# Performance work log

Hardware: AMD Instinct MI355X
Metric: run time of the kernel (lower is better)

Reference implementation:

```python
import jax, jax.numpy as jnp
import numpy as np

N = 8192; E = 131072; K = 20; IN_DIM = 3; HID = 256; N_CLASSES = 32


def setup_inputs():
    key = jax.random.key(0)
    ks = jax.random.split(key, 16)

    def w(k, shape):
        lim = 1.0 / np.sqrt(shape[0])
        return jax.random.uniform(k, shape, jnp.float32, -lim, lim)

    f32 = jnp.float32
    return {
        "features": jax.random.normal(ks[0], (N, IN_DIM), f32),
        "src": jax.random.randint(ks[1], (E,), 0, N, jnp.int32),
        "dst": jax.random.randint(ks[2], (E,), 0, N, jnp.int32),
        # GraphConv params
        "Wc1": w(ks[3], (IN_DIM, HID)), "bc1": jnp.zeros((HID,), f32),
        "Wc2": w(ks[4], (HID, HID)), "bc2": jnp.zeros((HID,), f32),
        "Wc3": w(ks[5], (64, N_CLASSES)), "bc3": jnp.zeros((N_CLASSES,), f32),
        # DynamicEdgeConv 1 MLP: [2*256 -> 256 -> 256], Linear+BN+ReLU each
        "W11": w(ks[6], (2 * HID, 256)), "b11": jnp.zeros((256,), f32), "g11": jnp.ones((256,), f32), "be11": jnp.zeros((256,), f32),
        "W12": w(ks[7], (256, 256)), "b12": jnp.zeros((256,), f32), "g12": jnp.ones((256,), f32), "be12": jnp.zeros((256,), f32),
        # DynamicEdgeConv 2 MLP: [2*256 -> 64 -> 64]
        "W21": w(ks[8], (2 * 256, 64)), "b21": jnp.zeros((64,), f32), "g21": jnp.ones((64,), f32), "be21": jnp.zeros((64,), f32),
        "W22": w(ks[9], (64, 64)), "b22": jnp.zeros((64,), f32), "g22": jnp.ones((64,), f32), "be22": jnp.zeros((64,), f32),
    }


def reference(features, src, dst, Wc1, bc1, Wc2, bc2, Wc3, bc3,
              W11, b11, g11, be11, W12, b12, g12, be12,
              W21, b21, g21, be21, W22, b22, g22, be22):
    n = features.shape[0]
    ones_e = jnp.ones(src.shape[0], features.dtype)
    # DGL GraphConv norm='both': deg clamped to min 1
    dout = jnp.clip(jax.ops.segment_sum(ones_e, src, num_segments=n), 1.0) ** -0.5
    din = jnp.clip(jax.ops.segment_sum(ones_e, dst, num_segments=n), 1.0) ** -0.5

    def gconv(x, W, b, act):
        agg = jax.ops.segment_sum((x * dout[:, None])[src], dst, num_segments=n)
        r = (agg * din[:, None]) @ W + b
        return jax.nn.relu(r) if act else r

    def bn(x, g, b):  # BatchNorm1d in training mode over all edge rows
        mu = jnp.mean(x, axis=(0, 1), keepdims=True)
        var = jnp.mean(jnp.square(x - mu), axis=(0, 1), keepdims=True)
        return (x - mu) * jax.lax.rsqrt(var + 1e-5) * g + b

    def edge_conv(x, layers):
        # dynamic kNN graph on current features (self included, dist 0)
        sq = jnp.sum(x * x, axis=-1)
        d = sq[:, None] + sq[None, :] - 2.0 * (x @ x.T)  # [N,N]
        idx = jax.lax.top_k(-d, K)[1]                    # [N,K]
        xi = x[:, None, :]
        e = jnp.concatenate([jnp.broadcast_to(xi, (n, K, x.shape[-1])), x[idx] - xi], axis=-1)  # [N,K,2F]
        for W, b, g, be in layers:
            e = jax.nn.relu(bn(e @ W + b, g, be))
        return jnp.max(e, axis=1)  # max aggregation over neighbors

    h = gconv(features, Wc1, bc1, True)                                   # [N,256]
    h = edge_conv(h, [(W11, b11, g11, be11), (W12, b12, g12, be12)])      # [N,256]
    h = gconv(h, Wc2, bc2, True)                                          # [N,256]
    h = edge_conv(h, [(W21, b21, g21, be21), (W22, b22, g22, be22)])      # [N,64]
    return gconv(h, Wc3, bc3, False)                                      # [N,32]
```

## Files before the change

kernel.cpp:

```cpp
#include <hip/hip_runtime.h>

#define NN 8192
#define NE 131072
#define KNN 20
#define CH 4096
#define GBM 128
#define GBN 128
#define GBK 64

typedef __attribute__((ext_vector_type(4))) float f32x4;
typedef __attribute__((ext_vector_type(8))) __bf16 bf16x8;

__global__ void k_zero(float* p, int n){
  int i = blockIdx.x*256 + threadIdx.x;
  if (i < n) p[i] = 0.f;
}
__global__ void k_zero_i(int* p, int n){
  int i = blockIdx.x*256 + threadIdx.x;
  if (i < n) p[i] = 0;
}

__device__ __forceinline__ unsigned short f2bf(float x){
  unsigned u = __float_as_uint(x);
  unsigned r = (u + 0x7fff + ((u >> 16) & 1)) >> 16;
  return (unsigned short)r;
}
__device__ __forceinline__ float bf2f(unsigned short h){
  return __uint_as_float((unsigned)h << 16);
}
__device__ __forceinline__ void gload16(const void* g, void* l){
  __builtin_amdgcn_global_load_lds(
      (const __attribute__((address_space(1))) void*)g,
      (__attribute__((address_space(3))) void*)l, 16, 0, 0);
}
__device__ __forceinline__ unsigned mapu(float v){
  unsigned b = __float_as_uint(v);
  return b ^ (((unsigned)((int)b >> 31)) | 0x80000000u);
}
__device__ __forceinline__ float unmapu(unsigned u){
  unsigned b = (u & 0x80000000u) ? (u ^ 0x80000000u) : ~u;
  return __uint_as_float(b);
}

__global__ void k_count(const int* __restrict__ src, const int* __restrict__ dst,
                        int* cs, int* cd){
  int e = blockIdx.x*256 + threadIdx.x;
  if (e < NE){ atomicAdd(&cs[src[e]], 1); atomicAdd(&cd[dst[e]], 1); }
}
__global__ void k_deg(const int* cs, const int* cd, float* dout, float* din){
  int i = blockIdx.x*256 + threadIdx.x;
  if (i < NN){
    dout[i] = rsqrtf((float)max(cs[i], 1));
    din[i]  = rsqrtf((float)max(cd[i], 1));
  }
}
__global__ void k_scan(const int* __restrict__ cnt, int* __restrict__ off){
  __shared__ int sh[256];
  __shared__ int carry;
  int tid = threadIdx.x;
  if (tid == 0) carry = 0;
  __syncthreads();
  for (int base = 0; base < NN; base += 256){
    int v = cnt[base + tid];
    int x = v;
    sh[tid] = x; __syncthreads();
    for (int o = 1; o < 256; o <<= 1){
      int y = (tid >= o) ? sh[tid - o] : 0;
      __syncthreads();
      x += y; sh[tid] = x;
      __syncthreads();
    }
    off[base + tid] = carry + x - v;
    __syncthreads();
    if (tid == 255){
      carry += x;
      if (base + 256 == NN) off[NN] = carry;
    }
    __syncthreads();
  }
}
__global__ void k_fill(const int* __restrict__ src, const int* __restrict__ dst,
                       const int* __restrict__ roff, int* cursor, int* csr){
  int e = blockIdx.x*256 + threadIdx.x;
  if (e < NE){
    int d = dst[e];
    int p = atomicAdd(&cursor[d], 1);
    csr[roff[d] + p] = src[e];
  }
}

__global__ void k_gconv1(const float* __restrict__ feat, const int* __restrict__ roff,
                         const int* __restrict__ csr, const float* __restrict__ dout,
                         const float* __restrict__ din, const float* __restrict__ Wc1,
                         const float* __restrict__ bc1, float* __restrict__ h1){
  int wid = threadIdx.x >> 6, lane = threadIdx.x & 63;
  int i = blockIdx.x*4 + wid;
  float a0=0.f, a1=0.f, a2=0.f;
  int beg = roff[i], end = roff[i+1];
  for (int t = beg + lane; t < end; t += 64){
    int s = csr[t]; float w = dout[s];
    a0 += feat[s*3+0]*w; a1 += feat[s*3+1]*w; a2 += feat[s*3+2]*w;
  }
  for (int m = 32; m; m >>= 1){
    a0 += __shfl_xor(a0, m); a1 += __shfl_xor(a1, m); a2 += __shfl_xor(a2, m);
  }
  float dn = din[i];
  a0 *= dn; a1 *= dn; a2 *= dn;
  for (int c = lane; c < 256; c += 64){
    float r = a0*Wc1[c] + a1*Wc1[256+c] + a2*Wc1[512+c] + bc1[c];
    h1[(size_t)i*256 + c] = fmaxf(r, 0.f);
  }
}

__global__ void k_sq(const float* __restrict__ X, float* __restrict__ sq){
  int wid = threadIdx.x >> 6, lane = threadIdx.x & 63;
  int i = blockIdx.x*4 + wid;
  float4 v = *(const float4*)&X[(size_t)i*256 + lane*4];
  float s = v.x*v.x + v.y*v.y + v.z*v.z + v.w*v.w;
  for (int m = 32; m; m >>= 1) s += __shfl_xor(s, m);
  if (lane == 0) sq[i] = s;
}

__global__ void k_split(const float* __restrict__ X, unsigned short* __restrict__ xcat){
  int row = blockIdx.x, c = threadIdx.x;
  float x = X[(size_t)row*256 + c];
  unsigned short h = f2bf(x);
  unsigned short lo = f2bf(x - bf2f(h));
  xcat[(size_t)row*512 + c] = h;
  xcat[(size_t)row*512 + 256 + c] = lo;
}

__global__ void k_wsplit(const float* __restrict__ W, unsigned short* __restrict__ Whi,
                         unsigned short* __restrict__ Wlo){
  int k = blockIdx.x, n = threadIdx.x;
  float x = W[(size_t)k*256 + n];
  unsigned short h = f2bf(x);
  Whi[(size_t)n*256 + k] = h;
  Wlo[(size_t)n*256 + k] = f2bf(x - bf2f(h));
}
__global__ void k_wsplit64(const float* __restrict__ W, unsigned short* __restrict__ Whi,
                           unsigned short* __restrict__ Wlo){
  int k = blockIdx.x, n = threadIdx.x;
  float x = W[(size_t)k*64 + n];
  unsigned short h = f2bf(x);
  Whi[(size_t)n*64 + k] = h;
  Wlo[(size_t)n*64 + k] = f2bf(x - bf2f(h));
}

__global__ __launch_bounds__(256)
void k_gram_mfma(const unsigned short* __restrict__ Xcat, const float* __restrict__ sq,
                 float* __restrict__ G, int r0){
  __shared__ unsigned short sA[GBM*GBK];
  __shared__ unsigned short sB[GBM*GBK];
  __shared__ float sqr[GBM];
  __shared__ float sqc[GBN];
  int tid = threadIdx.x;
  int lw = tid >> 6, l = tid & 63;
  int rbl = blockIdx.y*GBM;
  int rb = r0 + rbl;
  int cb = blockIdx.x*GBN;

  if (tid < GBM) sqr[tid] = sq[rb + tid];
  else if (tid < GBM + GBN) sqc[tid - GBM] = sq[cb + tid - GBM];

  int srow = l >> 3;
  int scol = (l & 7) ^ srow;
  const unsigned short* srcA[4];
  const unsigned short* srcB[4];
  char* dstA[4]; char* dstB[4];
  #pragma unroll
  for (int i = 0; i < 4; i++){
    int c = lw*4 + i;
    int row = c*8 + srow;
    srcA[i] = Xcat + (size_t)(rb + row)*512 + scol*8;
    srcB[i] = Xcat + (size_t)(cb + row)*512 + scol*8;
    dstA[i] = (char*)sA + c*1024;
    dstB[i] = (char*)sB + c*1024;
  }

  int wm = lw >> 1, wn = lw & 1;
  int fm = l & 15, kg = l >> 4;
  unsigned offA[4][2], offB[4][2];
  #pragma unroll
  for (int mf = 0; mf < 4; mf++){
    int rowa = wm*64 + mf*16 + fm;
    int rowb = wn*64 + mf*16 + fm;
    #pragma unroll
    for (int ks = 0; ks < 2; ks++){
      offA[mf][ks] = rowa*128 + (((unsigned)(ks*4 + kg) ^ (rowa & 7)))*16;
      offB[mf][ks] = rowb*128 + (((unsigned)(ks*4 + kg) ^ (rowb & 7)))*16;
    }
  }

  f32x4 acc[4][4];
  #pragma unroll
  for (int m = 0; m < 4; m++)
    #pragma unroll
    for (int n = 0; n < 4; n++) acc[m][n] = (f32x4){0.f,0.f,0.f,0.f};

  #pragma unroll
  for (int s = 0; s < 12; s++){
    int sec = s >> 2;
    int inner = (s & 3)*64;
    int cbA = (sec == 1 ? 256 : 0) + inner;
    int cbB = (sec == 2 ? 256 : 0) + inner;
    #pragma unroll
    for (int i = 0; i < 4; i++){
      gload16(srcA[i] + cbA, dstA[i]);
      gload16(srcB[i] + cbB, dstB[i]);
    }
    __syncthreads();
    #pragma unroll
    for (int ks = 0; ks < 2; ks++){
      bf16x8 a[4], b[4];
      #pragma unroll
      for (int mf = 0; mf < 4; mf++) a[mf] = *(const bf16x8*)((const char*)sA + offA[mf][ks]);
      #pragma unroll
      for (int nf = 0; nf < 4; nf++) b[nf] = *(const bf16x8*)((const char*)sB + offB[nf][ks]);
      #pragma unroll
      for (int mf = 0; mf < 4; mf++)
        #pragma unroll
        for (int nf = 0; nf < 4; nf++)
          acc[mf][nf] = __builtin_amdgcn_mfma_f32_16x16x32_bf16(a[mf], b[nf], acc[mf][nf], 0, 0, 0);
    }
    __syncthreads();
  }

  #pragma unroll
  for (int mf = 0; mf < 4; mf++){
    int lr0 = wm*64 + mf*16 + kg*4;
    #pragma unroll
    for (int nf = 0; nf < 4; nf++){
      int lc = wn*64 + nf*16 + fm;
      float sc = sqc[lc];
      #pragma unroll
      for (int r = 0; r < 4; r++)
        G[(size_t)(rbl + lr0 + r)*NN + cb + lc] = (sqr[lr0 + r] + sc) - 2.f*acc[mf][nf][r];
    }
  }
}

__global__ __launch_bounds__(256)
void k_topk(const float* __restrict__ G, int r0, int* __restrict__ idxo){
  int tid = threadIdx.x;
  int wid = tid >> 6, lane = tid & 63;
  int rl = blockIdx.x*4 + wid;
  int gr = r0 + rl;
  const float4* row4 = (const float4*)(G + (size_t)rl*NN);

  float kd0=INFINITY,kd1=INFINITY,kd2=INFINITY,kd3=INFINITY,kd4=INFINITY,
        kd5=INFINITY,kd6=INFINITY,kd7=INFINITY,kd8=INFINITY,kd9=INFINITY,
        kd10=INFINITY,kd11=INFINITY,kd12=INFINITY,kd13=INFINITY,kd14=INFINITY,
        kd15=INFINITY,kd16=INFINITY,kd17=INFINITY,kd18=INFINITY,kd19=INFINITY;
  int ki0=0x7fffffff,ki1=0x7fffffff,ki2=0x7fffffff,ki3=0x7fffffff,ki4=0x7fffffff,
      ki5=0x7fffffff,ki6=0x7fffffff,ki7=0x7fffffff,ki8=0x7fffffff,ki9=0x7fffffff,
      ki10=0x7fffffff,ki11=0x7fffffff,ki12=0x7fffffff,ki13=0x7fffffff,ki14=0x7fffffff,
      ki15=0x7fffffff,ki16=0x7fffffff,ki17=0x7fffffff,ki18=0x7fffffff,ki19=0x7fffffff;

#define ST(U) { bool sw = nk < kd##U; float tv = kd##U; int tq = ki##U; \
      if (sw){ kd##U = nk; ki##U = ni; nk = tv; ni = tq; } }
#define INSE(kc, jc) { if ((kc) < kd19){ float nk = (kc); int ni = (jc); \
      ST(0) ST(1) ST(2) ST(3) ST(4) ST(5) ST(6) ST(7) ST(8) ST(9) \
      ST(10) ST(11) ST(12) ST(13) ST(14) ST(15) ST(16) ST(17) ST(18) ST(19) } }

  float4 gc = row4[lane];
  #pragma unroll 1
  for (int o = 0; o < 32; o++){
    float4 g = gc;
    if (o < 31) gc = row4[lane + (o+1)*64];
    int jb = (lane + o*64)*4;
    float t19 = kd19;
    float mn = fminf(fminf(g.x, g.y), fminf(g.z, g.w));
    if (__any(mn < t19)){
      INSE(g.x, jb+0);
      INSE(g.y, jb+1);
      INSE(g.z, jb+2);
      INSE(g.w, jb+3);
    }
  }
#undef INSE
#undef ST

#define MV(A,B) { kd##A = kd##B; ki##A = ki##B; }
  #pragma unroll 1
  for (int r = 0; r < KNN; r++){
    float bv = kd0; int bi = ki0;
    #pragma unroll
    for (int mm = 32; mm; mm >>= 1){
      float ov = __shfl_xor(bv, mm); int oi = __shfl_xor(bi, mm);
      if (ov < bv || (ov == bv && oi < bi)){ bv = ov; bi = oi; }
    }
    if (ki0 == bi){
      MV(0,1) MV(1,2) MV(2,3) MV(3,4) MV(4,5) MV(5,6) MV(6,7) MV(7,8) MV(8,9) MV(9,10)
      MV(10,11) MV(11,12) MV(12,13) MV(13,14) MV(14,15) MV(15,16) MV(16,17) MV(17,18) MV(18,19)
      kd19 = INFINITY; ki19 = 0x7fffffff;
    }
    if (lane == 0) idxo[(size_t)gr*KNN + r] = bi;
  }
#undef MV
}

__global__ void k_wd(const float* __restrict__ W, float* __restrict__ Wd, int rows, int M){
  int t = blockIdx.x*256 + threadIdx.x;
  if (t < rows*M) Wd[t] = W[t] - W[rows*M + t];
}

__global__ __launch_bounds__(256)
void k_mm_mfma(const unsigned short* __restrict__ Xc, const unsigned short* __restrict__ Wthi,
               const unsigned short* __restrict__ Wtlo, const float* __restrict__ bias,
               float* __restrict__ C, int relu){
  int tid = threadIdx.x;
  int lw = tid >> 6, l = tid & 63;
  int wm = lw >> 1, wn = lw & 1;
  int fm = l & 15, kg = l >> 4;
  int rb = blockIdx.x*32;

  const unsigned short* aptr = Xc + (size_t)(rb + wm*16 + fm)*512 + kg*8;
  const unsigned short* bhi[8];
  const unsigned short* blo[8];
  float bz[8];
  #pragma unroll
  for (int nf = 0; nf < 8; nf++){
    int col = wn*128 + nf*16 + fm;
    bhi[nf] = Wthi + (size_t)col*256 + kg*8;
    blo[nf] = Wtlo + (size_t)col*256 + kg*8;
    bz[nf] = bias ? bias[col] : 0.f;
  }

  f32x4 acc[8];
  #pragma unroll
  for (int n = 0; n < 8; n++) acc[n] = (f32x4){0.f,0.f,0.f,0.f};

  #pragma unroll 1
  for (int sec = 0; sec < 3; sec++){
    int ka = (sec == 1) ? 256 : 0;
    int bsec = (sec == 2);
    #pragma unroll
    for (int st = 0; st < 8; st++){
      bf16x8 a = *(const bf16x8*)(aptr + ka + st*32);
      #pragma unroll
      for (int nf = 0; nf < 8; nf++){
        const unsigned short* bp = bsec ? blo[nf] : bhi[nf];
        bf16x8 b = *(const bf16x8*)(bp + st*32);
        acc[nf] = __builtin_amdgcn_mfma_f32_16x16x32_bf16(a, b, acc[nf], 0, 0, 0);
      }
    }
  }

  #pragma unroll
  for (int nf = 0; nf < 8; nf++){
    int col = wn*128 + nf*16 + fm;
    #pragma unroll
    for (int r = 0; r < 4; r++){
      int row = rb + wm*16 + kg*4 + r;
      float v = acc[nf][r] + bz[nf];
      if (relu) v = fmaxf(v, 0.f);
      C[(size_t)row*256 + col] = v;
    }
  }
}

__global__ __launch_bounds__(256)
void k_mm(const float* __restrict__ A, const float* __restrict__ B,
          const float* __restrict__ bias, float* __restrict__ Cout,
          int n, int Kd, int M, int relu){
  __shared__ float la[16][68], lb[16][68];
  int tid = threadIdx.x;
  int rb = blockIdx.y*64, cb = blockIdx.x*64;
  int lr = tid >> 2, lq = (tid & 3)*4;
  int ty = tid >> 4, tx = tid & 15;
  float acc[4][4] = {};
  for (int k0 = 0; k0 < Kd; k0 += 16){
    __syncthreads();
    #pragma unroll
    for (int u = 0; u < 4; u++){
      int k = k0 + lq + u;
      la[lq+u][lr] = (k < Kd) ? A[(size_t)(rb+lr)*Kd + k] : 0.f;
    }
    int kk = tid >> 4; int cc = (tid & 15)*4;
    #pragma unroll
    for (int u = 0; u < 4; u++){
      int c = cb + cc + u; int k = k0 + kk;
      lb[kk][cc+u] = (k < Kd && c < M) ? B[(size_t)k*M + c] : 0.f;
    }
    __syncthreads();
    #pragma unroll
    for (int k = 0; k < 16; k++){
      float4 a = *(const float4*)&la[k][ty*4];
      float4 b = *(const float4*)&lb[k][tx*4];
      float avv[4] = {a.x,a.y,a.z,a.w}, bvv[4] = {b.x,b.y,b.z,b.w};
      #pragma unroll
      for (int u = 0; u < 4; u++)
        #pragma unroll
        for (int v = 0; v < 4; v++) acc[u][v] += avv[u]*bvv[v];
    }
  }
  #pragma unroll
  for (int u = 0; u < 4; u++){
    int r = rb + ty*4 + u;
    #pragma unroll
    for (int v = 0; v < 4; v++){
      int c = cb + tx*4 + v;
      if (c < M){
        float x = acc[u][v] + (bias ? bias[c] : 0.f);
        if (relu) x = fmaxf(x, 0.f);
        Cout[(size_t)r*M + c] = x;
      }
    }
  }
}

template<int C>
__global__ __launch_bounds__(256)
void k_stats1(const float* __restrict__ A, const float* __restrict__ P,
              const int* __restrict__ idx, float* __restrict__ ssum, float* __restrict__ ssq){
  __shared__ int si[128], sj[128];
  int tid = threadIdx.x;
  int s0 = blockIdx.x*128;
  if (tid < 128){ si[tid] = (s0 + tid)/KNN; sj[tid] = idx[s0 + tid]; }
  __syncthreads();
  constexpr int MPAR = 256/C;
  int tc = tid % C, sr = tid / C;
  float s = 0.f, q = 0.f;
  for (int m = sr; m < 128; m += MPAR){
    float v = A[(size_t)si[m]*C + tc] + P[(size_t)sj[m]*C + tc];
    s += v; q += v*v;
  }
  if constexpr (MPAR > 1){
    __shared__ float rs[256], rq[256];
    rs[tid] = s; rq[tid] = q; __syncthreads();
    if (sr == 0){
      for (int u = 1; u < MPAR; u++){ s += rs[u*C + tc]; q += rq[u*C + tc]; }
    }
  }
  if (sr == 0){ atomicAdd(&ssum[tc], s); atomicAdd(&ssq[tc], q); }
}

__global__ void k_bn_final(const float* __restrict__ ssum, const float* __restrict__ ssq,
                           const float* __restrict__ g, const float* __restrict__ be,
                           float* __restrict__ sb, float* __restrict__ tb, int C, float invn){
  int c = threadIdx.x;
  if (c < C){
    float mu = ssum[c]*invn;
    float var = fmaxf(ssq[c]*invn - mu*mu, 0.f);
    float s = g[c]*rsqrtf(var + 1e-5f);
    sb[c] = s; tb[c] = be[c] - mu*s;
  }
}

__global__ __launch_bounds__(256, 2)
void k_edge_mfma(const float* __restrict__ A, const float* __restrict__ P,
                 const int* __restrict__ idx, const float* __restrict__ sb,
                 const float* __restrict__ tb, const unsigned short* __restrict__ Wthi,
                 const unsigned short* __restrict__ Wtlo, const float* __restrict__ bias,
                 unsigned* __restrict__ h2u, float* __restrict__ ssum, float* __restrict__ ssq){
  __shared__ unsigned short ehi[64*256];
  __shared__ unsigned short elo[64*256];
  __shared__ int sj[64];
  int tid = threadIdx.x;
  int lw = tid >> 6, l = tid & 63;
  int s0 = blockIdx.x*64;
  if (tid < 64) sj[tid] = idx[s0 + tid];
  float sbc = sb[tid], tbc = tb[tid];
  __syncthreads();

  #pragma unroll 1
  for (int g = 0; g < 8; g++){
    float va[8];
    #pragma unroll
    for (int u = 0; u < 8; u++){
      int it = g*8 + u;
      int i = (s0 + it)/KNN;
      int j = sj[it];
      va[u] = A[(size_t)i*256 + tid] + P[(size_t)j*256 + tid];
    }
    #pragma unroll
    for (int u = 0; u < 8; u++){
      int it = g*8 + u;
      float v = fmaxf(va[u]*sbc + tbc, 0.f);
      unsigned short h = f2bf(v);
      unsigned short lo = f2bf(v - bf2f(h));
      unsigned off = (unsigned)it*512 + (((unsigned)tid*2) ^ (((unsigned)it & 7) << 4));
      *(unsigned short*)((char*)ehi + off) = h;
      *(unsigned short*)((char*)elo + off) = lo;
    }
  }
  __syncthreads();

  int fm = l & 15, kg = l >> 4;
  const unsigned short* bhi[4];
  const unsigned short* blo[4];
  float bz[4];
  #pragma unroll
  for (int nf = 0; nf < 4; nf++){
    int col = lw*64 + nf*16 + fm;
    bhi[nf] = Wthi + (size_t)col*256 + kg*8;
    blo[nf] = Wtlo + (size_t)col*256 + kg*8;
    bz[nf] = bias[col];
  }

  f32x4 acc[4][4];
  #pragma unroll
  for (int m = 0; m < 4; m++)
    #pragma unroll
    for (int n = 0; n < 4; n++) acc[m][n] = (f32x4){0.f,0.f,0.f,0.f};

  #pragma unroll 1
  for (int sec = 0; sec < 3; sec++){
    const char* abase = (sec == 1) ? (const char*)elo : (const char*)ehi;
    int bsec = (sec == 2);
    #pragma unroll 1
    for (int st = 0; st < 8; st++){
      int g = st*4 + kg;
      bf16x8 a[4], b[4];
      #pragma unroll
      for (int mf = 0; mf < 4; mf++){
        int row = mf*16 + fm;
        a[mf] = *(const bf16x8*)(abase + row*512 + ((unsigned)(g ^ (row & 7)))*16);
      }
      #pragma unroll
      for (int nf = 0; nf < 4; nf++){
        const unsigned short* bp = bsec ? blo[nf] : bhi[nf];
        b[nf] = *(const bf16x8*)(bp + st*32);
      }
      #pragma unroll
      for (int mf = 0; mf < 4; mf++)
        #pragma unroll
        for (int nf = 0; nf < 4; nf++)
          acc[mf][nf] = __builtin_amdgcn_mfma_f32_16x16x32_bf16(a[mf], b[nf], acc[mf][nf], 0, 0, 0);
    }
  }

  float s4[4], q4[4];
  #pragma unroll
  for (int nf = 0; nf < 4; nf++){ s4[nf] = 0.f; q4[nf] = 0.f; }
  #pragma unroll
  for (int mf = 0; mf < 4; mf++){
    int gR = s0 + mf*16 + kg*4;
    int n0 = gR/20, n3 = (gR+3)/20;
    int kk = n3*20 - gR;
    #pragma unroll
    for (int nf = 0; nf < 4; nf++){
      int col = lw*64 + nf*16 + fm;
      float v0 = acc[mf][nf][0] + bz[nf];
      float v1 = acc[mf][nf][1] + bz[nf];
      float v2 = acc[mf][nf][2] + bz[nf];
      float v3 = acc[mf][nf][3] + bz[nf];
      s4[nf] += v0 + v1 + v2 + v3;
      q4[nf] += v0*v0 + v1*v1 + v2*v2 + v3*v3;
      if (n0 == n3){
        float m = fmaxf(fmaxf(v0, v1), fmaxf(v2, v3));
        atomicMax(&h2u[(size_t)n0*256 + col], mapu(m));
      } else {
        float lo = v0, hi = v3;
        if (1 < kk) lo = fmaxf(lo, v1); else hi = fmaxf(hi, v1);
        if (2 < kk) lo = fmaxf(lo, v2); else hi = fmaxf(hi, v2);
        atomicMax(&h2u[(size_t)n0*256 + col], mapu(lo));
        atomicMax(&h2u[(size_t)n3*256 + col], mapu(hi));
      }
    }
  }
  #pragma unroll
  for (int nf = 0; nf < 4; nf++){
    s4[nf] += __shfl_xor(s4[nf], 16); q4[nf] += __shfl_xor(q4[nf], 16);
    s4[nf] += __shfl_xor(s4[nf], 32); q4[nf] += __shfl_xor(q4[nf], 32);
  }
  if (kg == 0){
    #pragma unroll
    for (int nf = 0; nf < 4; nf++){
      int col = lw*64 + nf*16 + fm;
      atomicAdd(&ssum[col], s4[nf]);
      atomicAdd(&ssq[col], q4[nf]);
    }
  }
}

__global__ void k_h2final(const unsigned* __restrict__ h2u, const float* __restrict__ sb,
                          const float* __restrict__ tb, float* __restrict__ h2){
  int n = blockIdx.x, c = threadIdx.x;
  float x = unmapu(h2u[(size_t)n*256 + c]);
  h2[(size_t)n*256 + c] = fmaxf(sb[c]*x + tb[c], 0.f);
}

__global__ __launch_bounds__(256, 2)
void k_edge_mfma64(const float* __restrict__ A, const float* __restrict__ P,
                   const int* __restrict__ idx, const float* __restrict__ sb,
                   const float* __restrict__ tb, const unsigned short* __restrict__ Wthi,
                   const unsigned short* __restrict__ Wtlo, const float* __restrict__ bias,
                   float* __restrict__ out, float* __restrict__ ssum, float* __restrict__ ssq){
  __shared__ unsigned short ehi[128*64];
  __shared__ unsigned short elo[128*64];
  __shared__ int sj[128];
  int tid = threadIdx.x;
  int lw = tid >> 6, l = tid & 63;
  int s0 = blockIdx.x*128;
  if (tid < 128) sj[tid] = idx[s0 + tid];
  int col0 = tid & 63, rgrp = tid >> 6;
  float sbc = sb[col0], tbc = tb[col0];
  __syncthreads();

  #pragma unroll 1
  for (int g = 0; g < 4; g++){
    float va[8];
    #pragma unroll
    for (int u = 0; u < 8; u++){
      int it = (g*8 + u)*4 + rgrp;
      int i = (s0 + it)/KNN;
      int j = sj[it];
      va[u] = A[(size_t)i*64 + col0] + P[(size_t)j*64 + col0];
    }
    #pragma unroll
    for (int u = 0; u < 8; u++){
      int it = (g*8 + u)*4 + rgrp;
      float v = fmaxf(va[u]*sbc + tbc, 0.f);
      unsigned short h = f2bf(v);
      unsigned short lo = f2bf(v - bf2f(h));
      unsigned off = (unsigned)it*128 + (((unsigned)col0*2) ^ (((unsigned)it & 7) << 4));
      *(unsigned short*)((char*)ehi + off) = h;
      *(unsigned short*)((char*)elo + off) = lo;
    }
  }
  __syncthreads();

  int wm = lw >> 1, wn = lw & 1;
  int fm = l & 15, kg = l >> 4;
  const unsigned short* bhi[2];
  const unsigned short* blo[2];
  float bz[2];
  #pragma unroll
  for (int nf = 0; nf < 2; nf++){
    int col = wn*32 + nf*16 + fm;
    bhi[nf] = Wthi + (size_t)col*64 + kg*8;
    blo[nf] = Wtlo + (size_t)col*64 + kg*8;
    bz[nf] = bias[col];
  }

  f32x4 acc[4][2];
  #pragma unroll
  for (int m = 0; m < 4; m++)
    #pragma unroll
    for (int n = 0; n < 2; n++) acc[m][n] = (f32x4){0.f,0.f,0.f,0.f};

  #pragma unroll 1
  for (int sec = 0; sec < 3; sec++){
    const char* abase = (sec == 1) ? (const char*)elo : (const char*)ehi;
    int bsec = (sec == 2);
    #pragma unroll
    for (int ks = 0; ks < 2; ks++){
      int g = ks*4 + kg;
      bf16x8 a[4], b[2];
      #pragma unroll
      for (int mf = 0; mf < 4; mf++){
        int row = wm*64 + mf*16 + fm;
        a[mf] = *(const bf16x8*)(abase + row*128 + ((unsigned)(g ^ (row & 7)))*16);
      }
      #pragma unroll
      for (int nf = 0; nf < 2; nf++){
        const unsigned short* bp = bsec ? blo[nf] : bhi[nf];
        b[nf] = *(const bf16x8*)(bp + ks*32);
      }
      #pragma unroll
      for (int mf = 0; mf < 4; mf++)
        #pragma unroll
        for (int nf = 0; nf < 2; nf++)
          acc[mf][nf] = __builtin_amdgcn_mfma_f32_16x16x32_bf16(a[mf], b[nf], acc[mf][nf], 0, 0, 0);
    }
  }

  float s2[2], q2[2];
  #pragma unroll
  for (int nf = 0; nf < 2; nf++){ s2[nf] = 0.f; q2[nf] = 0.f; }
  #pragma unroll
  for (int mf = 0; mf < 4; mf++){
    #pragma unroll
    for (int nf = 0; nf < 2; nf++){
      int col = wn*32 + nf*16 + fm;
      #pragma unroll
      for (int r = 0; r < 4; r++){
        int row = s0 + wm*64 + mf*16 + kg*4 + r;
        float v = acc[mf][nf][r] + bz[nf];
        out[(size_t)row*64 + col] = v;
        s2[nf] += v; q2[nf] += v*v;
      }
    }
  }
  #pragma unroll
  for (int nf = 0; nf < 2; nf++){
    s2[nf] += __shfl_xor(s2[nf], 16); q2[nf] += __shfl_xor(q2[nf], 16);
    s2[nf] += __shfl_xor(s2[nf], 32); q2[nf] += __shfl_xor(q2[nf], 32);
  }
  if (kg == 0){
    #pragma unroll
    for (int nf = 0; nf < 2; nf++){
      int col = wn*32 + nf*16 + fm;
      atomicAdd(&ssum[col], s2[nf]);
      atomicAdd(&ssq[col], q2[nf]);
    }
  }
}

template<int C>
__global__ void k_maxpool(const float* __restrict__ X, const float* __restrict__ sb,
                          const float* __restrict__ tb, float* __restrict__ H){
  constexpr int NPB = 256/C;
  int node = blockIdx.x*NPB + threadIdx.x / C;
  int c = threadIdx.x % C;
  float s = sb[c], t = tb[c];
  float mx = 0.f;
  for (int k = 0; k < KNN; k++){
    float v = X[(size_t)(node*KNN + k)*C + c]*s + t;
    mx = fmaxf(mx, v);
  }
  H[(size_t)node*C + c] = mx;
}

template<int C>
__global__ void k_agg(const float* __restrict__ X, const int* __restrict__ roff,
                      const int* __restrict__ csr, const float* __restrict__ dout,
                      const float* __restrict__ din, float* __restrict__ XA){
  int i = blockIdx.x; int c = threadIdx.x;
  float acc = 0.f;
  int b = roff[i], e = roff[i+1];
  for (int t = b; t < e; t++){
    int s = csr[t];
    acc += X[(size_t)s*C + c]*dout[s];
  }
  XA[(size_t)i*C + c] = acc*din[i];
}

extern "C" void kernel_launch(void* const* d_in, const int* in_sizes, int n_in,
                              void* d_out, int out_size, void* d_ws, size_t ws_size,
                              hipStream_t stream){
  const float* feat = (const float*)d_in[0];
  const int*   src  = (const int*)d_in[1];
  const int*   dst  = (const int*)d_in[2];
  const float* Wc1  = (const float*)d_in[3];
  const float* bc1  = (const float*)d_in[4];
  const float* Wc2  = (const float*)d_in[5];
  const float* bc2  = (const float*)d_in[6];
  const float* Wc3  = (const float*)d_in[7];
  const float* bc3  = (const float*)d_in[8];
  const float* W11  = (const float*)d_in[9];
  const float* b11  = (const float*)d_in[10];
  const float* g11  = (const float*)d_in[11];
  const float* be11 = (const float*)d_in[12];
  const float* W12  = (const float*)d_in[13];
  const float* b12  = (const float*)d_in[14];
  const float* g12  = (const float*)d_in[15];
  const float* be12 = (const float*)d_in[16];
  const float* W21  = (const float*)d_in[17];
  const float* b21  = (const float*)d_in[18];
  const float* g21  = (const float*)d_in[19];
  const float* be21 = (const float*)d_in[20];
  const float* W22  = (const float*)d_in[21];
  const float* b22  = (const float*)d_in[22];
  const float* g22  = (const float*)d_in[23];
  const float* be22 = (const float*)d_in[24];
  float* out = (float*)d_out;

  char* w = (char*)d_ws; size_t off = 0;
  auto alloc = [&](size_t bytes)->void*{
    void* p = w + off;
    off += bytes; off = (off + 255) & ~(size_t)255;
    return p;
  };
  int* cnt_s  = (int*)alloc(NN*4);
  int* cnt_d  = (int*)alloc(NN*4);
  int* roff   = (int*)alloc((NN+1)*4);
  int* cursor = (int*)alloc(NN*4);
  int* csr    = (int*)alloc(NE*4);
  int* idx    = (int*)alloc((size_t)NN*KNN*4);
  float* dout = (float*)alloc(NN*4);
  float* din  = (float*)alloc(NN*4);
  float* sqv  = (float*)alloc(NN*4);
  float* h1   = (float*)alloc((size_t)NN*256*4);
  float* h2   = (float*)alloc((size_t)NN*256*4);
  float* h3   = (float*)alloc((size_t)NN*256*4);
  float* h4   = (float*)alloc((size_t)NN*64*4);
  float* xa   = (float*)alloc((size_t)NN*256*4);
  float* Abuf = (float*)alloc((size_t)NN*256*4);
  float* Pbuf = (float*)alloc((size_t)NN*256*4);
  float* Wd   = (float*)alloc(256*256*4);
  float* ssum = (float*)alloc(256*4);
  float* ssq  = (float*)alloc(256*4);
  float* sbn  = (float*)alloc(256*4);
  float* tbn  = (float*)alloc(256*4);
  unsigned* h2u = (unsigned*)alloc((size_t)NN*256*4);
  unsigned short* wthi = (unsigned short*)alloc(256*256*2);
  unsigned short* wtlo = (unsigned short*)alloc(256*256*2);
  unsigned short* wdhi = (unsigned short*)alloc(256*256*2);
  unsigned short* wdlo = (unsigned short*)alloc(256*256*2);
  unsigned short* wbhi = (unsigned short*)alloc(256*256*2);
  unsigned short* wblo = (unsigned short*)alloc(256*256*2);
  unsigned short* wchi = (unsigned short*)alloc(256*256*2);
  unsigned short* wclo = (unsigned short*)alloc(256*256*2);
  unsigned short* w64hi = (unsigned short*)alloc(64*64*2);
  unsigned short* w64lo = (unsigned short*)alloc(64*64*2);
  float* out2 = (float*)alloc((size_t)NN*KNN*256*4);
  float* gram = out2;
  unsigned short* xcat = (unsigned short*)(out2 + (size_t)CH*NN);
  (void)ws_size; (void)n_in; (void)in_sizes; (void)out_size;

  const float invn = 1.0f / (float)(NN*KNN);

  k_zero_i<<<32, 256, 0, stream>>>(cnt_s, NN);
  k_zero_i<<<32, 256, 0, stream>>>(cnt_d, NN);
  k_zero_i<<<32, 256, 0, stream>>>(cursor, NN);
  k_count<<<NE/256, 256, 0, stream>>>(src, dst, cnt_s, cnt_d);
  k_deg<<<32, 256, 0, stream>>>(cnt_s, cnt_d, dout, din);
  k_scan<<<1, 256, 0, stream>>>(cnt_d, roff);
  k_fill<<<NE/256, 256, 0, stream>>>(src, dst, roff, cursor, csr);

  k_gconv1<<<NN/4, 256, 0, stream>>>(feat, roff, csr, dout, din, Wc1, bc1, h1);

  k_sq<<<NN/4, 256, 0, stream>>>(h1, sqv);
  k_split<<<NN, 256, 0, stream>>>(h1, xcat);
  for (int r0 = 0; r0 < NN; r0 += CH){
    k_gram_mfma<<<dim3(NN/GBN, CH/GBM), 256, 0, stream>>>(xcat, sqv, gram, r0);
    k_topk<<<CH/4, 256, 0, stream>>>(gram, r0, idx);
  }
  k_wd<<<256, 256, 0, stream>>>(W11, Wd, 256, 256);
  k_wsplit<<<256, 256, 0, stream>>>(Wd, wdhi, wdlo);
  k_wsplit<<<256, 256, 0, stream>>>(W11 + 256*256, wbhi, wblo);
  k_wsplit<<<256, 256, 0, stream>>>(W12, wthi, wtlo);
  k_mm_mfma<<<NN/32, 256, 0, stream>>>(xcat, wdhi, wdlo, b11, Abuf, 0);
  k_mm_mfma<<<NN/32, 256, 0, stream>>>(xcat, wbhi, wblo, nullptr, Pbuf, 0);
  k_zero<<<2, 256, 0, stream>>>(ssum, 256); k_zero<<<2, 256, 0, stream>>>(ssq, 256);
  k_stats1<256><<<NN*KNN/128, 256, 0, stream>>>(Abuf, Pbuf, idx, ssum, ssq);
  k_bn_final<<<1, 256, 0, stream>>>(ssum, ssq, g11, be11, sbn, tbn, 256, invn);
  k_zero<<<2, 256, 0, stream>>>(ssum, 256); k_zero<<<2, 256, 0, stream>>>(ssq, 256);
  k_zero_i<<<NN, 256, 0, stream>>>((int*)h2u, NN*256);
  k_edge_mfma<<<NN*KNN/64, 256, 0, stream>>>(Abuf, Pbuf, idx, sbn, tbn, wthi, wtlo, b12, h2u, ssum, ssq);
  k_bn_final<<<1, 256, 0, stream>>>(ssum, ssq, g12, be12, sbn, tbn, 256, invn);
  k_h2final<<<NN, 256, 0, stream>>>(h2u, sbn, tbn, h2);

  k_agg<256><<<NN, 256, 0, stream>>>(h2, roff, csr, dout, din, xa);
  k_split<<<NN, 256, 0, stream>>>(xa, xcat);
  k_wsplit<<<256, 256, 0, stream>>>(Wc2, wchi, wclo);
  k_mm_mfma<<<NN/32, 256, 0, stream>>>(xcat, wchi, wclo, bc2, h3, 1);

  k_sq<<<NN/4, 256, 0, stream>>>(h3, sqv);
  k_split<<<NN, 256, 0, stream>>>(h3, xcat);
  for (int r0 = 0; r0 < NN; r0 += CH){
    k_gram_mfma<<<dim3(NN/GBN, CH/GBM), 256, 0, stream>>>(xcat, sqv, gram, r0);
    k_topk<<<CH/4, 256, 0, stream>>>(gram, r0, idx);
  }
  k_wd<<<64, 256, 0, stream>>>(W21, Wd, 256, 64);
  k_wsplit64<<<64, 64, 0, stream>>>(W22, w64hi, w64lo);
  k_mm<<<dim3(1, NN/64), 256, 0, stream>>>(h3, Wd, b21, Abuf, NN, 256, 64, 0);
  k_mm<<<dim3(1, NN/64), 256, 0, stream>>>(h3, W21 + 256*64, nullptr, Pbuf, NN, 256, 64, 0);
  k_zero<<<2, 256, 0, stream>>>(ssum, 256); k_zero<<<2, 256, 0, stream>>>(ssq, 256);
  k_stats1<64><<<NN*KNN/128, 256, 0, stream>>>(Abuf, Pbuf, idx, ssum, ssq);
  k_bn_final<<<1, 256, 0, stream>>>(ssum, ssq, g21, be21, sbn, tbn, 64, invn);
  k_zero<<<2, 256, 0, stream>>>(ssum, 256); k_zero<<<2, 256, 0, stream>>>(ssq, 256);
  k_edge_mfma64<<<NN*KNN/128, 256, 0, stream>>>(Abuf, Pbuf, idx, sbn, tbn, w64hi, w64lo, b22, out2, ssum, ssq);
  k_bn_final<<<1, 256, 0, stream>>>(ssum, ssq, g22, be22, sbn, tbn, 64, invn);
  k_maxpool<64><<<NN/4, 256, 0, stream>>>(out2, sbn, tbn, h4);

  k_agg<64><<<NN, 64, 0, stream>>>(h4, roff, csr, dout, din, xa);
  k_mm<<<dim3(1, NN/64), 256, 0, stream>>>(xa, Wc3, bc3, out, NN, 64, 32, 0);
}
```

Before: 1.413 ms.

## Fuse second edge-conv max-pool into MFMA epilogue via atomicMax; widen top-k scan

The second edge-conv kernel no longer writes its full per-edge output. It folds each group of four rows into per-node maxima with atomicMax on order-preserving unsigned keys, and a small finalize kernel then applies the BN affine transform and ReLU. This removes the large per-edge intermediate write and the max-pool re-read. It relies on the BN scale being non-negative so that max commutes with the affine map, and it adds atomic contention plus an extra zeroing pass. Separately, the top-k scan now processes two float4 loads per iteration, which halves the number of wave-vote checks and gives more loads in flight.

Result: no change. 1.430 ms (+1.1%).

```diff
diff --git a/kernel.cpp b/kernel.cpp
--- a/kernel.cpp
+++ b/kernel.cpp
@@ -263,19 +263,29 @@
       ST(0) ST(1) ST(2) ST(3) ST(4) ST(5) ST(6) ST(7) ST(8) ST(9) \
       ST(10) ST(11) ST(12) ST(13) ST(14) ST(15) ST(16) ST(17) ST(18) ST(19) } }
 
-  float4 gc = row4[lane];
+  float4 g0c = row4[lane];
+  float4 g1c = row4[lane + 64];
   #pragma unroll 1
-  for (int o = 0; o < 32; o++){
-    float4 g = gc;
-    if (o < 31) gc = row4[lane + (o+1)*64];
-    int jb = (lane + o*64)*4;
+  for (int o = 0; o < 16; o++){
+    float4 g0 = g0c, g1 = g1c;
+    if (o < 15){
+      g0c = row4[lane + (o+1)*128];
+      g1c = row4[lane + 64 + (o+1)*128];
+    }
+    int jb0 = (lane + o*128)*4;
+    int jb1 = (lane + 64 + o*128)*4;
     float t19 = kd19;
-    float mn = fminf(fminf(g.x, g.y), fminf(g.z, g.w));
+    float mn = fminf(fminf(fminf(g0.x, g0.y), fminf(g0.z, g0.w)),
+                     fminf(fminf(g1.x, g1.y), fminf(g1.z, g1.w)));
     if (__any(mn < t19)){
-      INSE(g.x, jb+0);
-      INSE(g.y, jb+1);
-      INSE(g.z, jb+2);
-      INSE(g.w, jb+3);
+      INSE(g0.x, jb0+0);
+      INSE(g0.y, jb0+1);
+      INSE(g0.z, jb0+2);
+      INSE(g0.w, jb0+3);
+      INSE(g1.x, jb1+0);
+      INSE(g1.y, jb1+1);
+      INSE(g1.z, jb1+2);
+      INSE(g1.w, jb1+3);
     }
   }
 #undef INSE
@@ -587,7 +597,7 @@
                    const int* __restrict__ idx, const float* __restrict__ sb,
                    const float* __restrict__ tb, const unsigned short* __restrict__ Wthi,
                    const unsigned short* __restrict__ Wtlo, const float* __restrict__ bias,
-                   float* __restrict__ out, float* __restrict__ ssum, float* __restrict__ ssq){
+                   unsigned* __restrict__ h4u, float* __restrict__ ssum, float* __restrict__ ssq){
   __shared__ unsigned short ehi[128*64];
   __shared__ unsigned short elo[128*64];
   __shared__ int sj[128];
@@ -672,15 +682,27 @@
   for (int nf = 0; nf < 2; nf++){ s2[nf] = 0.f; q2[nf] = 0.f; }
   #pragma unroll
   for (int mf = 0; mf < 4; mf++){
+    int gR = s0 + wm*64 + mf*16 + kg*4;
+    int n0 = gR/20, n3 = (gR+3)/20;
+    int kk = n3*20 - gR;
     #pragma unroll
     for (int nf = 0; nf < 2; nf++){
       int col = wn*32 + nf*16 + fm;
-      #pragma unroll
-      for (int r = 0; r < 4; r++){
-        int row = s0 + wm*64 + mf*16 + kg*4 + r;
-        float v = acc[mf][nf][r] + bz[nf];
-        out[(size_t)row*64 + col] = v;
-        s2[nf] += v; q2[nf] += v*v;
+      float v0 = acc[mf][nf][0] + bz[nf];
+      float v1 = acc[mf][nf][1] + bz[nf];
+      float v2 = acc[mf][nf][2] + bz[nf];
+      float v3 = acc[mf][nf][3] + bz[nf];
+      s2[nf] += v0 + v1 + v2 + v3;
+      q2[nf] += v0*v0 + v1*v1 + v2*v2 + v3*v3;
+      if (n0 == n3){
+        float m = fmaxf(fmaxf(v0, v1), fmaxf(v2, v3));
+        atomicMax(&h4u[(size_t)n0*64 + col], mapu(m));
+      } else {
+        float lo = v0, hi = v3;
+        if (1 < kk) lo = fmaxf(lo, v1); else hi = fmaxf(hi, v1);
+        if (2 < kk) lo = fmaxf(lo, v2); else hi = fmaxf(hi, v2);
+        atomicMax(&h4u[(size_t)n0*64 + col], mapu(lo));
+        atomicMax(&h4u[(size_t)n3*64 + col], mapu(hi));
       }
     }
   }
@@ -699,19 +721,11 @@
   }
 }
 
-template<int C>
-__global__ void k_maxpool(const float* __restrict__ X, const float* __restrict__ sb,
-                          const float* __restrict__ tb, float* __restrict__ H){
-  constexpr int NPB = 256/C;
-  int node = blockIdx.x*NPB + threadIdx.x / C;
-  int c = threadIdx.x % C;
-  float s = sb[c], t = tb[c];
-  float mx = 0.f;
-  for (int k = 0; k < KNN; k++){
-    float v = X[(size_t)(node*KNN + k)*C + c]*s + t;
-    mx = fmaxf(mx, v);
-  }
-  H[(size_t)node*C + c] = mx;
+__global__ void k_h4final(const unsigned* __restrict__ h4u, const float* __restrict__ sb,
+                          const float* __restrict__ tb, float* __restrict__ h4){
+  int n = blockIdx.x*4 + (threadIdx.x >> 6), c = threadIdx.x & 63;
+  float x = unmapu(h4u[(size_t)n*64 + c]);
+  h4[(size_t)n*64 + c] = fmaxf(sb[c]*x + tb[c], 0.f);
 }
 
 template<int C>
@@ -786,6 +800,7 @@
   float* sbn  = (float*)alloc(256*4);
   float* tbn  = (float*)alloc(256*4);
   unsigned* h2u = (unsigned*)alloc((size_t)NN*256*4);
+  unsigned* h4u = (unsigned*)alloc((size_t)NN*64*4);
   unsigned short* wthi = (unsigned short*)alloc(256*256*2);
   unsigned short* wtlo = (unsigned short*)alloc(256*256*2);
   unsigned short* wdhi = (unsigned short*)alloc(256*256*2);
@@ -796,9 +811,9 @@
   unsigned short* wclo = (unsigned short*)alloc(256*256*2);
   unsigned short* w64hi = (unsigned short*)alloc(64*64*2);
   unsigned short* w64lo = (unsigned short*)alloc(64*64*2);
-  float* out2 = (float*)alloc((size_t)NN*KNN*256*4);
-  float* gram = out2;
-  unsigned short* xcat = (unsigned short*)(out2 + (size_t)CH*NN);
+  float* scratch = (float*)alloc((size_t)NN*KNN*256*4);
+  float* gram = scratch;
+  unsigned short* xcat = (unsigned short*)(scratch + (size_t)CH*NN);
   (void)ws_size; (void)n_in; (void)in_sizes; (void)out_size;
 
   const float invn = 1.0f / (float)(NN*KNN);
@@ -853,9 +868,10 @@
   k_stats1<64><<<NN*KNN/128, 256, 0, stream>>>(Abuf, Pbuf, idx, ssum, ssq);
   k_bn_final<<<1, 256, 0, stream>>>(ssum, ssq, g21, be21, sbn, tbn, 64, invn);
   k_zero<<<2, 256, 0, stream>>>(ssum, 256); k_zero<<<2, 256, 0, stream>>>(ssq, 256);
-  k_edge_mfma64<<<NN*KNN/128, 256, 0, stream>>>(Abuf, Pbuf, idx, sbn, tbn, w64hi, w64lo, b22, out2, ssum, ssq);
+  k_zero_i<<<NN/4, 256, 0, stream>>>((int*)h4u, NN*64);
+  k_edge_mfma64<<<NN*KNN/128, 256, 0, stream>>>(Abuf, Pbuf, idx, sbn, tbn, w64hi, w64lo, b22, h4u, ssum, ssq);
   k_bn_final<<<1, 256, 0, stream>>>(ssum, ssq, g22, be22, sbn, tbn, 64, invn);
-  k_maxpool<64><<<NN/4, 256, 0, stream>>>(out2, sbn, tbn, h4);
+  k_h4final<<<NN/4, 256, 0, stream>>>(h4u, sbn, tbn, h4);
 
   k_agg<64><<<NN, 64, 0, stream>>>(h4, roff, csr, dout, din, xa);
   k_mm<<<dim3(1, NN/64), 256, 0, stream>>>(xa, Wc3, bc3, out, NN, 64, 32, 0);
```
